# Kernel tuning notes

Measured on AMD Instinct MI355X. Metric: run time of the kernel, lower is better.

Reference implementation:

```python
import jax, jax.numpy as jnp
import numpy as np

DIM_IN = 128; DIM_OUT = 128; DIM_X = 256; L = 256
BATCH = 8192; STD = 0.5; EPS = 1e-3; CRL = 1.0


def setup_inputs() -> dict:
    key = jax.random.key(0)
    ks = jax.random.split(key, 9)
    n = 2 * DIM_X + L
    # trainable params (as in torch __init__)
    X   = jax.random.normal(ks[0], (n, n)) * STD
    Y   = jax.random.normal(ks[1], (DIM_X, DIM_X)) * STD
    B2  = jax.random.normal(ks[2], (DIM_X, DIM_IN)) * STD
    C2  = jax.random.normal(ks[3], (DIM_OUT, DIM_X)) * STD
    D21 = jax.random.normal(ks[4], (DIM_OUT, L)) * STD
    D22 = jax.random.normal(ks[5], (DIM_OUT, DIM_IN)) * STD
    D12 = jax.random.normal(ks[6], (L, DIM_IN)) * STD
    # derived params per update_model_param (stored detached in the torch module)
    H = X.T @ X + EPS * jnp.eye(n)
    H11 = H[:DIM_X, :DIM_X]
    H21 = H[DIM_X:DIM_X + L, :DIM_X]
    H22 = H[DIM_X:DIM_X + L, DIM_X:DIM_X + L]
    H31 = H[DIM_X + L:, :DIM_X]
    H32 = H[DIM_X + L:, DIM_X:DIM_X + L]
    H33 = H[DIM_X + L:, DIM_X + L:]
    Fm  = H31
    B1  = H32
    E   = 0.5 * (H11 + CRL * H33 + Y - Y.T)
    Lam = 0.5 * jnp.diag(H22)            # positive diagonal of Lambda
    D11 = -jnp.tril(H22, -1)             # strictly lower triangular
    C1  = -H21
    x    = jax.random.normal(ks[7], (1, 1, DIM_X)) * 0.1   # internal state (broadcast over batch)
    u_in = jax.random.normal(ks[8], (BATCH, 1, DIM_IN))
    return {"u_in": u_in, "x": x, "Fm": Fm, "B1": B1, "B2": B2, "C1": C1,
            "C2": C2, "D11": D11, "D12": D12, "D21": D21, "D22": D22,
            "E": E, "Lam": Lam}


def ren_forward(u_in, x, Fm, B1, B2, C1, C2, D11, D12, D21, D22, E, Lam):
    batch = u_in.shape[0]
    l = Lam.shape[0]
    # per-step affine terms that do not depend on w (hoisted out of the loop)
    cx = jnp.einsum('li,aoi->l', C1, x)         # (l,)   x has leading dims (1,1)
    du = jnp.einsum('li,boi->lbo', D12, u_in)   # (l,B,1)
    eye = jnp.eye(l, dtype=u_in.dtype)
    w0 = jnp.zeros((batch, 1, l), u_in.dtype)

    # sequential forward substitution: D11 is strictly lower triangular, so
    # step i only reads w columns < i and writes column i.
    def step(w, inp):
        d11_i, lam_i, cx_i, du_i, e_i = inp
        v = cx_i + jnp.einsum('bol,l->bo', w, d11_i) + du_i   # (B,1)
        w = w + e_i * jnp.tanh(v / lam_i)[..., None]          # write column i
        return w, None

    w, _ = jax.lax.scan(step, w0, (D11, Lam, cx, du, eye))    # (B,1,l)

    Einv_T = jnp.linalg.inv(E).T
    x_new = (jnp.einsum('aoi,ji->aoj', x, Fm)
             + jnp.einsum('bol,jl->boj', w, B1)
             + jnp.einsum('boi,ji->boj', u_in, B2)) @ Einv_T  # (B,1,dim_x)
    y = x_new @ C2.T + w @ D21.T + u_in @ D22.T               # (B,1,dim_out)
    return y


def reference(u_in, x, Fm, B1, B2, C1, C2, D11, D12, D21, D22, E, Lam):
    return ren_forward(u_in, x, Fm, B1, B2, C1, C2, D11, D12, D21, D22, E, Lam)
```

## Files before the change

### kernel.cpp

```cpp
#include <hip/hip_runtime.h>
#include <utility>

#define NB 8192

template <typename F, size_t... I>
__device__ __forceinline__ void sfor_impl(F&& f, std::index_sequence<I...>) {
  (f(std::integral_constant<int, (int)I>{}), ...);
}
template <int N, typename F>
__device__ __forceinline__ void sfor(F&& f) {
  sfor_impl((F&&)f, std::make_index_sequence<N>{});
}

constexpr int coff(int li) {
  int o = 0;
  for (int j = 0; j < li; ++j) o += ((63 - j) + 3) & ~3;
  return o;
}
#define CPACK_STRIDE 2176

__device__ __forceinline__ float fast_rcp(float x) {
  float r = __builtin_amdgcn_rcpf(x);
  return r * (2.0f - x * r);
}

__device__ __forceinline__ float fast_tanh(float x) {
  const float e = __expf(2.0f * fminf(x, 40.0f));
  return 1.0f - 2.0f * fast_rcp(e + 1.0f);
}


__device__ void dev_prep(const float* __restrict__ x, const float* __restrict__ C1,
                         const float* __restrict__ Fm, const float* __restrict__ Lam,
                         float* __restrict__ cx, float* __restrict__ xF,
                         float* __restrict__ rLam, int t) {
  float s1 = 0.f, s2 = 0.f;
  for (int i = 0; i < 256; ++i) {
    const float xi = x[i];
    s1 += C1[t * 256 + i] * xi;
    s2 += Fm[t * 256 + i] * xi;
  }
  cx[t] = s1;
  xF[t] = s2;
  rLam[t] = 1.0f / Lam[t];
}

__device__ void dev_pack(const float* __restrict__ D11, float* __restrict__ cpack,
                         int t) {
  const int c = t >> 6;
  const int lane = t & 63;
  int off = 0;
  for (int li = 0; li < 63; ++li) {
    if (lane < 63 - li)
      cpack[c * CPACK_STRIDE + off + lane] =
          D11[(c * 64 + li + 1 + lane) * 256 + (c * 64 + li)];
    off += ((63 - li) + 3) & ~3;
  }
}

__device__ void dev_inv(const float* __restrict__ srcT, int ld,
                        float* __restrict__ dstT, int tid, int s0, int s1) {
  __shared__ float Pcols[128][20];
  __shared__ float MB[128][20];
  __shared__ float Ar[16][132];
  __shared__ float invD[16 * 20];
  const int ti = tid >> 5;
  const int tj = tid & 31;
  const int R = ti * 8, C = tj * 4;
  float a[8][4];
#pragma unroll
  for (int j = 0; j < 4; ++j)
#pragma unroll
    for (int g = 0; g < 2; ++g) {
      const float4 v = *(const float4*)&srcT[(C + j) * ld + (R + 4 * g)];
      a[4 * g + 0][j] = v.x; a[4 * g + 1][j] = v.y;
      a[4 * g + 2][j] = v.z; a[4 * g + 3][j] = v.w;
    }

  for (int s = s0; s < s1; ++s) {
    if ((tj >> 2) == s) {
      const int c0 = C - 16 * s;
#pragma unroll
      for (int i = 0; i < 8; ++i)
        *(float4*)&Pcols[R + i][c0] =
            make_float4(a[i][0], a[i][1], a[i][2], a[i][3]);
    }
    if ((ti >> 1) == s) {
      const int r0 = R - 16 * s;
#pragma unroll
      for (int i = 0; i < 8; ++i)
        *(float4*)&Ar[r0 + i][C] =
            make_float4(a[i][0], a[i][1], a[i][2], a[i][3]);
    }
    __syncthreads();

    if (tid < 16) {
      float q[16];
#pragma unroll
      for (int g = 0; g < 4; ++g) {
        const float4 v = *(const float4*)&Pcols[s * 16 + tid][4 * g];
        q[4 * g] = v.x; q[4 * g + 1] = v.y; q[4 * g + 2] = v.z; q[4 * g + 3] = v.w;
      }
#pragma unroll
      for (int kk = 0; kk < 16; ++kk) {
        float ps[16];
#pragma unroll
        for (int j = 0; j < 16; ++j)
          ps[j] = __int_as_float(
              __builtin_amdgcn_readlane(__float_as_int(q[j]), kk));
        const float piv = fast_rcp(ps[kk]);
#pragma unroll
        for (int j = 0; j < 16; ++j) ps[j] = (j == kk) ? piv : ps[j] * piv;
        const bool isP = (tid == kk);
        const float te = isP ? -1.0f : q[kk];
#pragma unroll
        for (int j = 0; j < 16; ++j) {
          const float base = (isP || j == kk) ? 0.0f : q[j];
          q[j] = base - te * ps[j];
        }
      }
#pragma unroll
      for (int g = 0; g < 4; ++g)
        *(float4*)&invD[tid * 20 + 4 * g] =
            make_float4(q[4 * g], q[4 * g + 1], q[4 * g + 2], q[4 * g + 3]);
    }
    __syncthreads();

    {
      const int r = tid & 127, h = tid >> 7;
      float4 mv;
      if ((r >> 4) == s) {
        mv = *(const float4*)&invD[(r & 15) * 20 + 4 * h];
      } else {
        mv = make_float4(0.f, 0.f, 0.f, 0.f);
#pragma unroll
        for (int g = 0; g < 4; ++g) {
          const float4 p = *(const float4*)&Pcols[r][4 * g];
          const float pc[4] = {p.x, p.y, p.z, p.w};
#pragma unroll
          for (int q = 0; q < 4; ++q) {
            const float4 d = *(const float4*)&invD[(4 * g + q) * 20 + 4 * h];
            mv.x -= pc[q] * d.x; mv.y -= pc[q] * d.y;
            mv.z -= pc[q] * d.z; mv.w -= pc[q] * d.w;
          }
        }
      }
      *(float4*)&MB[r][4 * h] = mv;
    }
    __syncthreads();

    if ((tj >> 2) == s) {
      const int c0 = C - 16 * s;
#pragma unroll
      for (int i = 0; i < 8; ++i) {
        const float4 m = *(const float4*)&MB[R + i][c0];
        a[i][0] = m.x; a[i][1] = m.y; a[i][2] = m.z; a[i][3] = m.w;
      }
    } else {
      if ((ti >> 1) == s) {
#pragma unroll
        for (int i = 0; i < 8; ++i)
#pragma unroll
          for (int j = 0; j < 4; ++j) a[i][j] = 0.f;
      }
#pragma unroll
      for (int half = 0; half < 2; ++half) {
        float4 ar[8];
#pragma unroll
        for (int k = 0; k < 8; ++k)
          ar[k] = *(const float4*)&Ar[half * 8 + k][C];
#pragma unroll
        for (int i = 0; i < 8; ++i) {
          const float4 m0 = *(const float4*)&MB[R + i][half * 8];
          const float4 m1 = *(const float4*)&MB[R + i][half * 8 + 4];
          const float mi[8] = {m0.x, m0.y, m0.z, m0.w, m1.x, m1.y, m1.z, m1.w};
#pragma unroll
          for (int k = 0; k < 8; ++k) {
            a[i][0] += mi[k] * ar[k].x;
            a[i][1] += mi[k] * ar[k].y;
            a[i][2] += mi[k] * ar[k].z;
            a[i][3] += mi[k] * ar[k].w;
          }
        }
      }
    }
    __syncthreads();
  }
#pragma unroll
  for (int j = 0; j < 4; ++j)
#pragma unroll
    for (int g = 0; g < 2; ++g)
      *(float4*)&dstT[(C + j) * 128 + (R + 4 * g)] = make_float4(
          a[4 * g + 0][j], a[4 * g + 1][j], a[4 * g + 2][j], a[4 * g + 3][j]);
}

__device__ void dev_T(const float* __restrict__ u, float* __restrict__ vw, int bid,
                      int t) {
  __shared__ float buf[64 * 65];
  const int b0 = bid * 64;
#pragma unroll
  for (int h = 0; h < 2; ++h) {
#pragma unroll
    for (int q = 0; q < 8; ++q) {
      const int idx = q * 512 + t;
      const int bl = idx >> 6;
      const int i2 = idx & 63;
      buf[i2 * 65 + bl] = u[(b0 + bl) * 128 + 64 * h + i2];
    }
    __syncthreads();
#pragma unroll
    for (int q = 0; q < 8; ++q) {
      const int idx = q * 512 + t;
      const int i2 = idx >> 6;
      const int bl = idx & 63;
      vw[(256 + 64 * h + i2) * NB + b0 + bl] = buf[i2 * 65 + bl];
    }
    __syncthreads();
  }
}

__device__ void dev_du512(const float* __restrict__ D12, const float* __restrict__ cx,
                          float* __restrict__ vw, int bid, int t) {
  __shared__ float4 ut[8][256];
  __shared__ float Dl[16 * 128];
  const int bx = bid & 7;
  const int l0 = (bid >> 3) * 16;
  const int tt = t & 255;
  const int lh = t >> 8;
#pragma unroll
  for (int q = 0; q < 4; ++q) {
    const int e = q * 512 + t;
    Dl[e] = D12[(l0 + (e >> 7)) * 128 + (e & 127)];
  }
  const float4* vw4 = (const float4*)vw;
  float4* vw4o = (float4*)vw;
  const int b4 = bx * 256 + tt;
  float4 acc[8];
#pragma unroll
  for (int j = 0; j < 8; ++j) {
    const float cj = cx[l0 + lh * 8 + j];
    acc[j] = make_float4(cj, cj, cj, cj);
  }
  for (int kc = 0; kc < 16; ++kc) {
    __syncthreads();
#pragma unroll
    for (int q = 0; q < 4; ++q) {
      const int e = q * 512 + t;
      ut[e >> 8][e & 255] =
          vw4[(256 + kc * 8 + (e >> 8)) * 2048 + bx * 256 + (e & 255)];
    }
    __syncthreads();
#pragma unroll
    for (int i2 = 0; i2 < 8; ++i2) {
      const float4 w = ut[i2][tt];
#pragma unroll
      for (int j = 0; j < 8; ++j) {
        const float d = Dl[(lh * 8 + j) * 128 + kc * 8 + i2];
        acc[j].x += d * w.x;
        acc[j].y += d * w.y;
        acc[j].z += d * w.z;
        acc[j].w += d * w.w;
      }
    }
  }
#pragma unroll
  for (int j = 0; j < 8; ++j) vw4o[(l0 + lh * 8 + j) * 2048 + b4] = acc[j];
}

__device__ void dev_WZ(const float* __restrict__ E, const float* __restrict__ C2,
                       const float* __restrict__ inv1T, float* __restrict__ W,
                       float* __restrict__ z1, int gid) {
  const int half = gid >> 14;
  const int idx = gid & 16383;
  const int j = idx >> 7;
  const int i = idx & 127;
  float s = 0.f;
  if (half == 0) {
    for (int m = 0; m < 128; ++m) s += inv1T[m * 128 + i] * E[(128 + j) * 256 + m];
    W[i * 128 + j] = s;
  } else {
    for (int m = 0; m < 128; ++m) s += inv1T[m * 128 + i] * C2[j * 256 + m];
    z1[i * 128 + j] = s;
  }
}

__device__ void dev_SC(const float* __restrict__ E, const float* __restrict__ C2,
                       const float* __restrict__ W, const float* __restrict__ z1,
                       float* __restrict__ STt, float* __restrict__ c2p, int gid) {
  if (gid < 16384) {
    const int jj = gid >> 7;
    const int i = gid & 127;
    float s = E[(128 + jj) * 256 + 128 + i];
    for (int m = 0; m < 128; ++m) s -= E[m * 256 + 128 + i] * W[m * 128 + jj];
    STt[jj * 128 + i] = s;
  } else {
    const int idx = gid - 16384;
    const int i = idx >> 7;
    const int o = idx & 127;
    float s = C2[o * 256 + 128 + i];
    for (int m = 0; m < 128; ++m) s -= E[m * 256 + 128 + i] * z1[m * 128 + o];
    c2p[i * 128 + o] = s;
  }
}

__device__ void dev_G2(const float* __restrict__ inv2T, const float* __restrict__ c2p,
                       float* __restrict__ g2, int gid) {
  const int i = gid >> 7;
  const int o = gid & 127;
  float s = 0.f;
  for (int m = 0; m < 128; ++m) s += inv2T[m * 128 + i] * c2p[m * 128 + o];
  g2[i * 128 + o] = s;
}

__device__ void dev_G1(const float* __restrict__ W, const float* __restrict__ z1,
                       const float* __restrict__ g2, float* __restrict__ g1, int gid) {
  const int i = gid >> 7;
  const int o = gid & 127;
  float s = z1[i * 128 + o];
  for (int m = 0; m < 128; ++m) s -= W[i * 128 + m] * g2[m * 128 + o];
  g1[i * 128 + o] = s;
}

__device__ void dev_R(const float* __restrict__ B1, const float* __restrict__ B2,
                      const float* __restrict__ D21, const float* __restrict__ D22,
                      const float* __restrict__ g1, const float* __restrict__ g2,
                      const float* __restrict__ xF, float* __restrict__ R,
                      float* __restrict__ y0, int gid) {
  if (gid < 32768) {
    const int o = gid >> 8;
    const int l = gid & 255;
    float s = D21[o * 256 + l];
    for (int m = 0; m < 128; ++m) {
      s += g1[m * 128 + o] * B1[m * 256 + l];
      s += g2[m * 128 + o] * B1[(128 + m) * 256 + l];
    }
    R[o * 384 + l] = s;
  } else if (gid < 49152) {
    const int t2 = gid - 32768;
    const int o = t2 >> 7;
    const int i = t2 & 127;
    float s = D22[o * 128 + i];
    for (int m = 0; m < 128; ++m) {
      s += g1[m * 128 + o] * B2[m * 128 + i];
      s += g2[m * 128 + o] * B2[(128 + m) * 128 + i];
    }
    R[o * 384 + 256 + i] = s;
  } else if (gid < 49280) {
    const int o = gid - 49152;
    float s = 0.f;
    for (int m = 0; m < 128; ++m) {
      s += g1[m * 128 + o] * xF[m];
      s += g2[m * 128 + o] * xF[128 + m];
    }
    y0[o] = s;
  }
}

__device__ void dev_scan(const float* __restrict__ cpack,
                         const float* __restrict__ rLam, float* __restrict__ vw,
                         int c, int bid, int t) {
  __shared__ float sc[CPACK_STRIDE];
  __shared__ float srl[64];
  for (int i = t; i < CPACK_STRIDE; i += 512) sc[i] = cpack[c * CPACK_STRIDE + i];
  if (t < 64) srl[t] = rLam[c * 64 + t];
  __syncthreads();
  if (t >= 256) return;

  const int b = bid * 256 + t;
  const int l0 = c * 64;
  const float4* cp4 = (const float4*)sc;
  float v[64];
#pragma unroll
  for (int li = 0; li < 64; ++li) v[li] = vw[(l0 + li) * NB + b];
  sfor<64>([&](auto LI) {
    constexpr int li = decltype(LI)::value;
    const float w = fast_tanh(v[li] * srl[li]);
    vw[(l0 + li) * NB + b] = w;
    constexpr int n = 63 - li;
    constexpr int off4 = coff(li) / 4;
    sfor<(n + 3) / 4>([&](auto Q) {
      constexpr int q = decltype(Q)::value;
      const float4 d = cp4[off4 + q];
      if constexpr (4 * q + 0 < n) v[li + 1 + 4 * q + 0] += d.x * w;
      if constexpr (4 * q + 1 < n) v[li + 1 + 4 * q + 1] += d.y * w;
      if constexpr (4 * q + 2 < n) v[li + 1 + 4 * q + 2] += d.z * w;
      if constexpr (4 * q + 3 < n) v[li + 1 + 4 * q + 3] += d.w * w;
    });
  });
}

__device__ void dev_upd(const float* __restrict__ D11, float* __restrict__ vw, int c,
                        int role, int lane) {
  float4* vw4 = (float4*)vw;
  const int b4 = (role & 7) * 256 + lane;
  const int lp0 = (c + 1) * 64 + (role >> 3) * 8;
  const int k0 = c * 64;
  float4 acc[8];
#pragma unroll
  for (int j = 0; j < 8; ++j) acc[j] = vw4[(lp0 + j) * 2048 + b4];
  for (int k = 0; k < 64; ++k) {
    const float4 wv = vw4[(k0 + k) * 2048 + b4];
#pragma unroll
    for (int j = 0; j < 8; ++j) {
      const float d = D11[(lp0 + j) * 256 + k0 + k];
      acc[j].x += d * wv.x;
      acc[j].y += d * wv.y;
      acc[j].z += d * wv.z;
      acc[j].w += d * wv.w;
    }
  }
#pragma unroll
  for (int j = 0; j < 8; ++j) vw4[(lp0 + j) * 2048 + b4] = acc[j];
}


__global__ __launch_bounds__(512) void mega1(const float* u, const float* x,
                                             const float* C1, const float* Fm,
                                             const float* Lam, const float* D11,
                                             const float* E, float* vw, float* cx,
                                             float* xF, float* rLam, float* cpack,
                                             float* invSt) {
  const int bid = blockIdx.x;
  const int t = threadIdx.x;
  if (bid < 128) {
    dev_T(u, vw, bid, t);
  } else if (bid == 128) {
    if (t < 256) dev_prep(x, C1, Fm, Lam, cx, xF, rLam, t);
  } else if (bid == 129) {
    if (t < 256) dev_pack(D11, cpack, t);
  } else {
    dev_inv(E, 256, invSt, t, 0, 4);
  }
}

__global__ __launch_bounds__(512) void mega2(const float* D12, const float* cx,
                                             float* vw, const float* invSt,
                                             float* inv1T) {
  const int bid = blockIdx.x;
  const int t = threadIdx.x;
  if (bid < 128) dev_du512(D12, cx, vw, bid, t);
  else dev_inv(invSt, 128, inv1T, t, 4, 8);
}

__global__ __launch_bounds__(512) void mega3(const float* cpack, const float* rLam,
                                             float* vw, const float* E,
                                             const float* C2, const float* inv1T,
                                             float* W, float* z1) {
  const int bid = blockIdx.x;
  const int t = threadIdx.x;
  if (bid < 32) {
    dev_scan(cpack, rLam, vw, 0, bid, t);
  } else {
    dev_WZ(E, C2, inv1T, W, z1, (bid - 32) * 512 + t);
  }
}

__global__ __launch_bounds__(512) void mega4(const float* D11, float* vw,
                                             const float* E, const float* C2,
                                             const float* W, const float* z1,
                                             float* STt, float* c2p) {
  const int bid = blockIdx.x;
  const int t = threadIdx.x;
  if (bid < 96) dev_upd(D11, vw, 0, bid * 2 + (t >> 8), t & 255);
  else dev_SC(E, C2, W, z1, STt, c2p, (bid - 96) * 512 + t);
}

__global__ __launch_bounds__(512) void mega5(const float* cpack, const float* rLam,
                                             float* vw, const float* STt,
                                             float* inv2St) {
  const int bid = blockIdx.x;
  const int t = threadIdx.x;
  if (bid < 32) {
    dev_scan(cpack, rLam, vw, 1, bid, t);
  } else {
    dev_inv(STt, 128, inv2St, t, 0, 4);
  }
}

__global__ __launch_bounds__(512) void mega6(const float* D11, float* vw,
                                             const float* inv2St, float* inv2T) {
  const int bid = blockIdx.x;
  const int t = threadIdx.x;
  if (bid < 64) dev_upd(D11, vw, 1, bid * 2 + (t >> 8), t & 255);
  else dev_inv(inv2St, 128, inv2T, t, 4, 8);
}

__global__ __launch_bounds__(512) void mega7(const float* cpack, const float* rLam,
                                             float* vw, const float* inv2T,
                                             const float* c2p, float* g2) {
  const int bid = blockIdx.x;
  const int t = threadIdx.x;
  if (bid < 32) {
    dev_scan(cpack, rLam, vw, 2, bid, t);
  } else {
    dev_G2(inv2T, c2p, g2, (bid - 32) * 512 + t);
  }
}

__global__ __launch_bounds__(512) void mega8(const float* D11, float* vw,
                                             const float* W, const float* z1,
                                             const float* g2, float* g1) {
  const int bid = blockIdx.x;
  const int t = threadIdx.x;
  if (bid < 32) dev_upd(D11, vw, 2, bid * 2 + (t >> 8), t & 255);
  else dev_G1(W, z1, g2, g1, (bid - 32) * 512 + t);
}

__global__ __launch_bounds__(512) void mega9(const float* cpack, const float* rLam,
                                             float* vw, const float* B1,
                                             const float* B2, const float* D21,
                                             const float* D22, const float* g1,
                                             const float* g2, const float* xF,
                                             float* R, float* y0) {
  const int bid = blockIdx.x;
  const int t = threadIdx.x;
  if (bid < 32) {
    dev_scan(cpack, rLam, vw, 3, bid, t);
  } else {
    dev_R(B1, B2, D21, D22, g1, g2, xF, R, y0, (bid - 32) * 512 + t);
  }
}

__global__ __launch_bounds__(512) void k_y(const float* __restrict__ vw,
                                           const float* __restrict__ R,
                                           const float* __restrict__ y0,
                                           float* __restrict__ y) {
  __shared__ float Rl[1536];
  __shared__ float part[256 * 16];
  const int tid = threadIdx.x;
  const int bid = blockIdx.x;
  const int gx = bid & 7;
  const int gy = bid >> 3;
  const int o0 = gy * 4;
#pragma unroll
  for (int q = 0; q < 3; ++q) Rl[q * 512 + tid] = R[o0 * 384 + q * 512 + tid];
  __syncthreads();

  const int lane = tid & 255;
  const int ks = tid >> 8;
  const int kbase = ks * 192;
  const float4* vw4 = (const float4*)vw;
  const int b4 = gx * 256 + lane;
  float acc[4][4];
#pragma unroll
  for (int j = 0; j < 4; ++j)
#pragma unroll
    for (int bi = 0; bi < 4; ++bi) acc[bi][j] = 0.f;

  for (int k = 0; k < 192; k += 8) {
    float4 w[8];
#pragma unroll
    for (int kk = 0; kk < 8; ++kk) w[kk] = vw4[(kbase + k + kk) * 2048 + b4];
#pragma unroll
    for (int j = 0; j < 4; ++j) {
      const float4 r0 = *(const float4*)&Rl[j * 384 + kbase + k];
      const float4 r1 = *(const float4*)&Rl[j * 384 + kbase + k + 4];
      acc[0][j] += r0.x * w[0].x + r0.y * w[1].x + r0.z * w[2].x + r0.w * w[3].x +
                   r1.x * w[4].x + r1.y * w[5].x + r1.z * w[6].x + r1.w * w[7].x;
      acc[1][j] += r0.x * w[0].y + r0.y * w[1].y + r0.z * w[2].y + r0.w * w[3].y +
                   r1.x * w[4].y + r1.y * w[5].y + r1.z * w[6].y + r1.w * w[7].y;
      acc[2][j] += r0.x * w[0].z + r0.y * w[1].z + r0.z * w[2].z + r0.w * w[3].z +
                   r1.x * w[4].z + r1.y * w[5].z + r1.z * w[6].z + r1.w * w[7].z;
      acc[3][j] += r0.x * w[0].w + r0.y * w[1].w + r0.z * w[2].w + r0.w * w[3].w +
                   r1.x * w[4].w + r1.y * w[5].w + r1.z * w[6].w + r1.w * w[7].w;
    }
  }

  if (ks == 1) {
#pragma unroll
    for (int bi = 0; bi < 4; ++bi)
      *(float4*)&part[lane * 16 + bi * 4] =
          make_float4(acc[bi][0], acc[bi][1], acc[bi][2], acc[bi][3]);
  }
  __syncthreads();
  if (ks == 0) {
    const int b0 = b4 * 4;
#pragma unroll
    for (int bi = 0; bi < 4; ++bi) {
      const float4 p = *(const float4*)&part[lane * 16 + bi * 4];
      *(float4*)&y[(b0 + bi) * 128 + o0] =
          make_float4(acc[bi][0] + p.x + y0[o0 + 0],
                      acc[bi][1] + p.y + y0[o0 + 1],
                      acc[bi][2] + p.z + y0[o0 + 2],
                      acc[bi][3] + p.w + y0[o0 + 3]);
    }
  }
}

extern "C" void kernel_launch(void* const* d_in, const int* in_sizes, int n_in,
                              void* d_out, int out_size, void* d_ws, size_t ws_size,
                              hipStream_t stream) {
  const float* u   = (const float*)d_in[0];
  const float* x   = (const float*)d_in[1];
  const float* Fm  = (const float*)d_in[2];
  const float* B1  = (const float*)d_in[3];
  const float* B2  = (const float*)d_in[4];
  const float* C1  = (const float*)d_in[5];
  const float* C2  = (const float*)d_in[6];
  const float* D11 = (const float*)d_in[7];
  const float* D12 = (const float*)d_in[8];
  const float* D21 = (const float*)d_in[9];
  const float* D22 = (const float*)d_in[10];
  const float* E   = (const float*)d_in[11];
  const float* Lam = (const float*)d_in[12];
  float* y = (float*)d_out;

  float* F = (float*)d_ws;
  float* vw    = F;
  float* SMb   = F + 384 * NB;
  float* inv1T = SMb;
  float* Wm    = SMb + 16384;
  float* z1    = SMb + 32768;
  float* STt   = SMb + 49152;
  float* c2p   = SMb + 65536;
  float* inv2T = SMb + 81920;
  float* g2    = SMb + 98304;
  float* g1    = SMb + 114688;
  float* Rm    = SMb + 131072;
  float* y0v   = SMb + 180224;
  float* cx    = SMb + 180352;
  float* xF    = SMb + 180608;
  float* rLam  = SMb + 180864;
  float* cpack = SMb + 181120;
  float* invSt  = STt;
  float* inv2St = g1;

  mega1<<<131, 512, 0, stream>>>(u, x, C1, Fm, Lam, D11, E, vw, cx, xF, rLam,
                                 cpack, invSt);
  mega2<<<129, 512, 0, stream>>>(D12, cx, vw, invSt, inv1T);
  mega3<<<96, 512, 0, stream>>>(cpack, rLam, vw, E, C2, inv1T, Wm, z1);
  mega4<<<160, 512, 0, stream>>>(D11, vw, E, C2, Wm, z1, STt, c2p);
  mega5<<<33, 512, 0, stream>>>(cpack, rLam, vw, STt, inv2St);
  mega6<<<65, 512, 0, stream>>>(D11, vw, inv2St, inv2T);
  mega7<<<64, 512, 0, stream>>>(cpack, rLam, vw, inv2T, c2p, g2);
  mega8<<<64, 512, 0, stream>>>(D11, vw, Wm, z1, g2, g1);
  mega9<<<129, 512, 0, stream>>>(cpack, rLam, vw, B1, B2, D21, D22, g1, g2, xF,
                                 Rm, y0v);
  k_y<<<256, 512, 0, stream>>>(vw, Rm, y0v, y);
}
```

Before: 302.3 us.

## Merge ten stage kernels into one cooperative kernel with grid syncs

Replaces the chain of ten separate kernel launches with one cooperative persistent kernel of 256 blocks that separates stages with grid.sync, and moves all per-function shared arrays into one shared buffer. The block matrix inversion is rescheduled across more stages so it overlaps the scan/update chain. This is meant to remove launch gaps and inter-kernel drain between the many short dependent stages. In exchange, every block must wait at all twelve grid barriers, and the kernel needs all 256 blocks of 512 threads resident at the same time.

Measured after the change: 1.129 ms. +273.4%, slower.

```diff
diff --git a/kernel.cpp b/kernel.cpp
--- a/kernel.cpp
+++ b/kernel.cpp
@@ -1,5 +1,8 @@
 #include <hip/hip_runtime.h>
+#include <hip/hip_cooperative_groups.h>
 #include <utility>
+
+namespace cg = cooperative_groups;
 
 #define NB 8192
 
@@ -58,12 +61,12 @@
   }
 }
 
-__device__ void dev_inv(const float* __restrict__ srcT, int ld,
-                        float* __restrict__ dstT, int tid, int s0, int s1) {
-  __shared__ float Pcols[128][20];
-  __shared__ float MB[128][20];
-  __shared__ float Ar[16][132];
-  __shared__ float invD[16 * 20];
+__device__ void dev_inv(float* __restrict__ sm, const float* __restrict__ srcT,
+                        int ld, float* __restrict__ dstT, int tid, int s0, int s1) {
+  float* PC = sm;
+  float* MBp = sm + 2560;
+  float* AR = sm + 5120;
+  float* IV = sm + 7232;
   const int ti = tid >> 5;
   const int tj = tid & 31;
   const int R = ti * 8, C = tj * 4;
@@ -82,14 +85,14 @@
       const int c0 = C - 16 * s;
 #pragma unroll
       for (int i = 0; i < 8; ++i)
-        *(float4*)&Pcols[R + i][c0] =
+        *(float4*)&PC[(R + i) * 20 + c0] =
             make_float4(a[i][0], a[i][1], a[i][2], a[i][3]);
     }
     if ((ti >> 1) == s) {
       const int r0 = R - 16 * s;
 #pragma unroll
       for (int i = 0; i < 8; ++i)
-        *(float4*)&Ar[r0 + i][C] =
+        *(float4*)&AR[(r0 + i) * 132 + C] =
             make_float4(a[i][0], a[i][1], a[i][2], a[i][3]);
     }
     __syncthreads();
@@ -98,7 +101,7 @@
       float q[16];
 #pragma unroll
       for (int g = 0; g < 4; ++g) {
-        const float4 v = *(const float4*)&Pcols[s * 16 + tid][4 * g];
+        const float4 v = *(const float4*)&PC[(s * 16 + tid) * 20 + 4 * g];
         q[4 * g] = v.x; q[4 * g + 1] = v.y; q[4 * g + 2] = v.z; q[4 * g + 3] = v.w;
       }
 #pragma unroll
@@ -121,7 +124,7 @@
       }
 #pragma unroll
       for (int g = 0; g < 4; ++g)
-        *(float4*)&invD[tid * 20 + 4 * g] =
+        *(float4*)&IV[tid * 20 + 4 * g] =
             make_float4(q[4 * g], q[4 * g + 1], q[4 * g + 2], q[4 * g + 3]);
     }
     __syncthreads();
@@ -130,22 +133,22 @@
       const int r = tid & 127, h = tid >> 7;
       float4 mv;
       if ((r >> 4) == s) {
-        mv = *(const float4*)&invD[(r & 15) * 20 + 4 * h];
+        mv = *(const float4*)&IV[(r & 15) * 20 + 4 * h];
       } else {
         mv = make_float4(0.f, 0.f, 0.f, 0.f);
 #pragma unroll
         for (int g = 0; g < 4; ++g) {
-          const float4 p = *(const float4*)&Pcols[r][4 * g];
+          const float4 p = *(const float4*)&PC[r * 20 + 4 * g];
           const float pc[4] = {p.x, p.y, p.z, p.w};
 #pragma unroll
           for (int q = 0; q < 4; ++q) {
-            const float4 d = *(const float4*)&invD[(4 * g + q) * 20 + 4 * h];
+            const float4 d = *(const float4*)&IV[(4 * g + q) * 20 + 4 * h];
             mv.x -= pc[q] * d.x; mv.y -= pc[q] * d.y;
             mv.z -= pc[q] * d.z; mv.w -= pc[q] * d.w;
           }
         }
       }
-      *(float4*)&MB[r][4 * h] = mv;
+      *(float4*)&MBp[r * 20 + 4 * h] = mv;
     }
     __syncthreads();
 
@@ -153,7 +156,7 @@
       const int c0 = C - 16 * s;
 #pragma unroll
       for (int i = 0; i < 8; ++i) {
-        const float4 m = *(const float4*)&MB[R + i][c0];
+        const float4 m = *(const float4*)&MBp[(R + i) * 20 + c0];
         a[i][0] = m.x; a[i][1] = m.y; a[i][2] = m.z; a[i][3] = m.w;
       }
     } else {
@@ -168,11 +171,11 @@
         float4 ar[8];
 #pragma unroll
         for (int k = 0; k < 8; ++k)
-          ar[k] = *(const float4*)&Ar[half * 8 + k][C];
+          ar[k] = *(const float4*)&AR[(half * 8 + k) * 132 + C];
 #pragma unroll
         for (int i = 0; i < 8; ++i) {
-          const float4 m0 = *(const float4*)&MB[R + i][half * 8];
-          const float4 m1 = *(const float4*)&MB[R + i][half * 8 + 4];
+          const float4 m0 = *(const float4*)&MBp[(R + i) * 20 + half * 8];
+          const float4 m1 = *(const float4*)&MBp[(R + i) * 20 + half * 8 + 4];
           const float mi[8] = {m0.x, m0.y, m0.z, m0.w, m1.x, m1.y, m1.z, m1.w};
 #pragma unroll
           for (int k = 0; k < 8; ++k) {
@@ -194,9 +197,8 @@
           a[4 * g + 0][j], a[4 * g + 1][j], a[4 * g + 2][j], a[4 * g + 3][j]);
 }
 
-__device__ void dev_T(const float* __restrict__ u, float* __restrict__ vw, int bid,
-                      int t) {
-  __shared__ float buf[64 * 65];
+__device__ void dev_T(float* __restrict__ sm, const float* __restrict__ u,
+                      float* __restrict__ vw, int bid, int t) {
   const int b0 = bid * 64;
 #pragma unroll
   for (int h = 0; h < 2; ++h) {
@@ -205,7 +207,7 @@
       const int idx = q * 512 + t;
       const int bl = idx >> 6;
       const int i2 = idx & 63;
-      buf[i2 * 65 + bl] = u[(b0 + bl) * 128 + 64 * h + i2];
+      sm[i2 * 65 + bl] = u[(b0 + bl) * 128 + 64 * h + i2];
     }
     __syncthreads();
 #pragma unroll
@@ -213,16 +215,17 @@
       const int idx = q * 512 + t;
       const int i2 = idx >> 6;
       const int bl = idx & 63;
-      vw[(256 + 64 * h + i2) * NB + b0 + bl] = buf[i2 * 65 + bl];
-    }
-    __syncthreads();
-  }
-}
-
-__device__ void dev_du512(const float* __restrict__ D12, const float* __restrict__ cx,
-                          float* __restrict__ vw, int bid, int t) {
-  __shared__ float4 ut[8][256];
-  __shared__ float Dl[16 * 128];
+      vw[(256 + 64 * h + i2) * NB + b0 + bl] = sm[i2 * 65 + bl];
+    }
+    __syncthreads();
+  }
+}
+
+__device__ void dev_du512(float* __restrict__ sm, const float* __restrict__ D12,
+                          const float* __restrict__ cx, float* __restrict__ vw,
+                          int bid, int t) {
+  float4* ut4 = (float4*)sm;
+  float* Dl = sm + 8192;
   const int bx = bid & 7;
   const int l0 = (bid >> 3) * 16;
   const int tt = t & 255;
@@ -246,13 +249,13 @@
 #pragma unroll
     for (int q = 0; q < 4; ++q) {
       const int e = q * 512 + t;
-      ut[e >> 8][e & 255] =
+      ut4[(e >> 8) * 256 + (e & 255)] =
           vw4[(256 + kc * 8 + (e >> 8)) * 2048 + bx * 256 + (e & 255)];
     }
     __syncthreads();
 #pragma unroll
     for (int i2 = 0; i2 < 8; ++i2) {
-      const float4 w = ut[i2][tt];
+      const float4 w = ut4[i2 * 256 + tt];
 #pragma unroll
       for (int j = 0; j < 8; ++j) {
         const float d = Dl[(lh * 8 + j) * 128 + kc * 8 + i2];
@@ -356,37 +359,38 @@
   }
 }
 
-__device__ void dev_scan(const float* __restrict__ cpack,
+__device__ void dev_scan(float* __restrict__ sm, const float* __restrict__ cpack,
                          const float* __restrict__ rLam, float* __restrict__ vw,
                          int c, int bid, int t) {
-  __shared__ float sc[CPACK_STRIDE];
-  __shared__ float srl[64];
+  float* sc = sm;
+  float* srl = sm + CPACK_STRIDE;
   for (int i = t; i < CPACK_STRIDE; i += 512) sc[i] = cpack[c * CPACK_STRIDE + i];
   if (t < 64) srl[t] = rLam[c * 64 + t];
   __syncthreads();
-  if (t >= 256) return;
-
-  const int b = bid * 256 + t;
-  const int l0 = c * 64;
-  const float4* cp4 = (const float4*)sc;
-  float v[64];
-#pragma unroll
-  for (int li = 0; li < 64; ++li) v[li] = vw[(l0 + li) * NB + b];
-  sfor<64>([&](auto LI) {
-    constexpr int li = decltype(LI)::value;
-    const float w = fast_tanh(v[li] * srl[li]);
-    vw[(l0 + li) * NB + b] = w;
-    constexpr int n = 63 - li;
-    constexpr int off4 = coff(li) / 4;
-    sfor<(n + 3) / 4>([&](auto Q) {
-      constexpr int q = decltype(Q)::value;
-      const float4 d = cp4[off4 + q];
-      if constexpr (4 * q + 0 < n) v[li + 1 + 4 * q + 0] += d.x * w;
-      if constexpr (4 * q + 1 < n) v[li + 1 + 4 * q + 1] += d.y * w;
-      if constexpr (4 * q + 2 < n) v[li + 1 + 4 * q + 2] += d.z * w;
-      if constexpr (4 * q + 3 < n) v[li + 1 + 4 * q + 3] += d.w * w;
+  if (t < 256) {
+    const int b = bid * 256 + t;
+    const int l0 = c * 64;
+    const float4* cp4 = (const float4*)sc;
+    float v[64];
+#pragma unroll
+    for (int li = 0; li < 64; ++li) v[li] = vw[(l0 + li) * NB + b];
+    sfor<64>([&](auto LI) {
+      constexpr int li = decltype(LI)::value;
+      const float w = fast_tanh(v[li] * srl[li]);
+      vw[(l0 + li) * NB + b] = w;
+      constexpr int n = 63 - li;
+      constexpr int off4 = coff(li) / 4;
+      sfor<(n + 3) / 4>([&](auto Q) {
+        constexpr int q = decltype(Q)::value;
+        const float4 d = cp4[off4 + q];
+        if constexpr (4 * q + 0 < n) v[li + 1 + 4 * q + 0] += d.x * w;
+        if constexpr (4 * q + 1 < n) v[li + 1 + 4 * q + 1] += d.y * w;
+        if constexpr (4 * q + 2 < n) v[li + 1 + 4 * q + 2] += d.z * w;
+        if constexpr (4 * q + 3 < n) v[li + 1 + 4 * q + 3] += d.w * w;
+      });
     });
-  });
+  }
+  __syncthreads();
 }
 
 __device__ void dev_upd(const float* __restrict__ D11, float* __restrict__ vw, int c,
@@ -413,122 +417,11 @@
   for (int j = 0; j < 8; ++j) vw4[(lp0 + j) * 2048 + b4] = acc[j];
 }
 
-
-__global__ __launch_bounds__(512) void mega1(const float* u, const float* x,
-                                             const float* C1, const float* Fm,
-                                             const float* Lam, const float* D11,
-                                             const float* E, float* vw, float* cx,
-                                             float* xF, float* rLam, float* cpack,
-                                             float* invSt) {
-  const int bid = blockIdx.x;
-  const int t = threadIdx.x;
-  if (bid < 128) {
-    dev_T(u, vw, bid, t);
-  } else if (bid == 128) {
-    if (t < 256) dev_prep(x, C1, Fm, Lam, cx, xF, rLam, t);
-  } else if (bid == 129) {
-    if (t < 256) dev_pack(D11, cpack, t);
-  } else {
-    dev_inv(E, 256, invSt, t, 0, 4);
-  }
-}
-
-__global__ __launch_bounds__(512) void mega2(const float* D12, const float* cx,
-                                             float* vw, const float* invSt,
-                                             float* inv1T) {
-  const int bid = blockIdx.x;
-  const int t = threadIdx.x;
-  if (bid < 128) dev_du512(D12, cx, vw, bid, t);
-  else dev_inv(invSt, 128, inv1T, t, 4, 8);
-}
-
-__global__ __launch_bounds__(512) void mega3(const float* cpack, const float* rLam,
-                                             float* vw, const float* E,
-                                             const float* C2, const float* inv1T,
-                                             float* W, float* z1) {
-  const int bid = blockIdx.x;
-  const int t = threadIdx.x;
-  if (bid < 32) {
-    dev_scan(cpack, rLam, vw, 0, bid, t);
-  } else {
-    dev_WZ(E, C2, inv1T, W, z1, (bid - 32) * 512 + t);
-  }
-}
-
-__global__ __launch_bounds__(512) void mega4(const float* D11, float* vw,
-                                             const float* E, const float* C2,
-                                             const float* W, const float* z1,
-                                             float* STt, float* c2p) {
-  const int bid = blockIdx.x;
-  const int t = threadIdx.x;
-  if (bid < 96) dev_upd(D11, vw, 0, bid * 2 + (t >> 8), t & 255);
-  else dev_SC(E, C2, W, z1, STt, c2p, (bid - 96) * 512 + t);
-}
-
-__global__ __launch_bounds__(512) void mega5(const float* cpack, const float* rLam,
-                                             float* vw, const float* STt,
-                                             float* inv2St) {
-  const int bid = blockIdx.x;
-  const int t = threadIdx.x;
-  if (bid < 32) {
-    dev_scan(cpack, rLam, vw, 1, bid, t);
-  } else {
-    dev_inv(STt, 128, inv2St, t, 0, 4);
-  }
-}
-
-__global__ __launch_bounds__(512) void mega6(const float* D11, float* vw,
-                                             const float* inv2St, float* inv2T) {
-  const int bid = blockIdx.x;
-  const int t = threadIdx.x;
-  if (bid < 64) dev_upd(D11, vw, 1, bid * 2 + (t >> 8), t & 255);
-  else dev_inv(inv2St, 128, inv2T, t, 4, 8);
-}
-
-__global__ __launch_bounds__(512) void mega7(const float* cpack, const float* rLam,
-                                             float* vw, const float* inv2T,
-                                             const float* c2p, float* g2) {
-  const int bid = blockIdx.x;
-  const int t = threadIdx.x;
-  if (bid < 32) {
-    dev_scan(cpack, rLam, vw, 2, bid, t);
-  } else {
-    dev_G2(inv2T, c2p, g2, (bid - 32) * 512 + t);
-  }
-}
-
-__global__ __launch_bounds__(512) void mega8(const float* D11, float* vw,
-                                             const float* W, const float* z1,
-                                             const float* g2, float* g1) {
-  const int bid = blockIdx.x;
-  const int t = threadIdx.x;
-  if (bid < 32) dev_upd(D11, vw, 2, bid * 2 + (t >> 8), t & 255);
-  else dev_G1(W, z1, g2, g1, (bid - 32) * 512 + t);
-}
-
-__global__ __launch_bounds__(512) void mega9(const float* cpack, const float* rLam,
-                                             float* vw, const float* B1,
-                                             const float* B2, const float* D21,
-                                             const float* D22, const float* g1,
-                                             const float* g2, const float* xF,
-                                             float* R, float* y0) {
-  const int bid = blockIdx.x;
-  const int t = threadIdx.x;
-  if (bid < 32) {
-    dev_scan(cpack, rLam, vw, 3, bid, t);
-  } else {
-    dev_R(B1, B2, D21, D22, g1, g2, xF, R, y0, (bid - 32) * 512 + t);
-  }
-}
-
-__global__ __launch_bounds__(512) void k_y(const float* __restrict__ vw,
-                                           const float* __restrict__ R,
-                                           const float* __restrict__ y0,
-                                           float* __restrict__ y) {
-  __shared__ float Rl[1536];
-  __shared__ float part[256 * 16];
-  const int tid = threadIdx.x;
-  const int bid = blockIdx.x;
+__device__ void dev_ky(float* __restrict__ sm, const float* __restrict__ vw,
+                       const float* __restrict__ R, const float* __restrict__ y0,
+                       float* __restrict__ y, int bid, int tid) {
+  float* Rl = sm;
+  float* part = sm + 1536;
   const int gx = bid & 7;
   const int gy = bid >> 3;
   const int o0 = gy * 4;
@@ -585,6 +478,75 @@
                       acc[bi][3] + p.w + y0[o0 + 3]);
     }
   }
+}
+
+__global__ __launch_bounds__(512) void megacoop(
+    const float* __restrict__ u, const float* __restrict__ x,
+    const float* __restrict__ Fm, const float* __restrict__ B1,
+    const float* __restrict__ B2, const float* __restrict__ C1,
+    const float* __restrict__ C2, const float* __restrict__ D11,
+    const float* __restrict__ D12, const float* __restrict__ D21,
+    const float* __restrict__ D22, const float* __restrict__ E,
+    const float* __restrict__ Lam, float* __restrict__ y, float* vw,
+    float* inv1T, float* Wm, float* z1, float* STt, float* c2p, float* inv2T,
+    float* g2, float* g1, float* Rm, float* y0v, float* cx, float* xF,
+    float* rLam, float* cpack, float* invSt, float* inv2St) {
+  __shared__ __align__(16) float sm[10240];
+  cg::grid_group grid = cg::this_grid();
+  const int B = blockIdx.x;
+  const int t = threadIdx.x;
+
+  if (B < 128) {
+    dev_T(sm, u, vw, B, t);
+  } else if (B == 255) {
+    if (t < 256) dev_prep(x, C1, Fm, Lam, cx, xF, rLam, t);
+    if (t < 256) dev_pack(D11, cpack, t);
+    dev_inv(sm, E, 256, invSt, t, 0, 2);
+  }
+  __threadfence(); grid.sync();
+
+  if (B < 128) dev_du512(sm, D12, cx, vw, B, t);
+  else if (B == 255) dev_inv(sm, invSt, 128, invSt, t, 2, 4);
+  __threadfence(); grid.sync();
+
+  if (B < 32) dev_scan(sm, cpack, rLam, vw, 0, B, t);
+  else if (B == 255) dev_inv(sm, invSt, 128, invSt, t, 4, 6);
+  __threadfence(); grid.sync();
+
+  if (B < 96) dev_upd(D11, vw, 0, B * 2 + (t >> 8), t & 255);
+  else if (B == 255) dev_inv(sm, invSt, 128, inv1T, t, 6, 8);
+  __threadfence(); grid.sync();
+
+  if (B < 32) dev_scan(sm, cpack, rLam, vw, 1, B, t);
+  else if (B < 96) dev_WZ(E, C2, inv1T, Wm, z1, (B - 32) * 512 + t);
+  __threadfence(); grid.sync();
+
+  if (B < 64) dev_upd(D11, vw, 1, B * 2 + (t >> 8), t & 255);
+  else if (B < 128) dev_SC(E, C2, Wm, z1, STt, c2p, (B - 64) * 512 + t);
+  __threadfence(); grid.sync();
+
+  if (B < 32) dev_scan(sm, cpack, rLam, vw, 2, B, t);
+  else if (B == 255) dev_inv(sm, STt, 128, inv2St, t, 0, 3);
+  __threadfence(); grid.sync();
+
+  if (B < 32) dev_upd(D11, vw, 2, B * 2 + (t >> 8), t & 255);
+  else if (B == 255) dev_inv(sm, inv2St, 128, inv2St, t, 3, 6);
+  __threadfence(); grid.sync();
+
+  if (B < 32) dev_scan(sm, cpack, rLam, vw, 3, B, t);
+  else if (B == 255) dev_inv(sm, inv2St, 128, inv2T, t, 6, 8);
+  __threadfence(); grid.sync();
+
+  if (B < 32) dev_G2(inv2T, c2p, g2, B * 512 + t);
+  __threadfence(); grid.sync();
+
+  if (B < 32) dev_G1(Wm, z1, g2, g1, B * 512 + t);
+  __threadfence(); grid.sync();
+
+  if (B < 97) dev_R(B1, B2, D21, D22, g1, g2, xF, Rm, y0v, B * 512 + t);
+  __threadfence(); grid.sync();
+
+  dev_ky(sm, vw, Rm, y0v, y, B, t);
 }
 
 extern "C" void kernel_launch(void* const* d_in, const int* in_sizes, int n_in,
@@ -625,16 +587,14 @@
   float* invSt  = STt;
   float* inv2St = g1;
 
-  mega1<<<131, 512, 0, stream>>>(u, x, C1, Fm, Lam, D11, E, vw, cx, xF, rLam,
-                                 cpack, invSt);
-  mega2<<<129, 512, 0, stream>>>(D12, cx, vw, invSt, inv1T);
-  mega3<<<96, 512, 0, stream>>>(cpack, rLam, vw, E, C2, inv1T, Wm, z1);
-  mega4<<<160, 512, 0, stream>>>(D11, vw, E, C2, Wm, z1, STt, c2p);
-  mega5<<<33, 512, 0, stream>>>(cpack, rLam, vw, STt, inv2St);
-  mega6<<<65, 512, 0, stream>>>(D11, vw, inv2St, inv2T);
-  mega7<<<64, 512, 0, stream>>>(cpack, rLam, vw, inv2T, c2p, g2);
-  mega8<<<64, 512, 0, stream>>>(D11, vw, Wm, z1, g2, g1);
-  mega9<<<129, 512, 0, stream>>>(cpack, rLam, vw, B1, B2, D21, D22, g1, g2, xF,
-                                 Rm, y0v);
-  k_y<<<256, 512, 0, stream>>>(vw, Rm, y0v, y);
-}
+  void* args[] = {(void*)&u,    (void*)&x,     (void*)&Fm,   (void*)&B1,
+                  (void*)&B2,   (void*)&C1,    (void*)&C2,   (void*)&D11,
+                  (void*)&D12,  (void*)&D21,   (void*)&D22,  (void*)&E,
+                  (void*)&Lam,  (void*)&y,     (void*)&vw,   (void*)&inv1T,
+                  (void*)&Wm,   (void*)&z1,    (void*)&STt,  (void*)&c2p,
+                  (void*)&inv2T,(void*)&g2,    (void*)&g1,   (void*)&Rm,
+                  (void*)&y0v,  (void*)&cx,    (void*)&xF,   (void*)&rLam,
+                  (void*)&cpack,(void*)&invSt, (void*)&inv2St};
+  hipLaunchCooperativeKernel((const void*)megacoop, dim3(256), dim3(512), args,
+                             0, stream);
+}
```
